# Optimization experiments

Measured on AMD Instinct MI355X. Metric: run time of the kernel, lower is better.

The kernel has to match this reference:

```python
import jax, jax.numpy as jnp
import numpy as np

NB, H, NH, R, C, V, B = 4, 256, 8, 20, 128, 32, 2
P = R * (R - 1) // 2  # 190 pairs


def _pair_matrix(rows):
    # each row of the mask has exactly two ones (a row pair); equals torch.combinations scatter
    i, j = np.triu_indices(rows, k=1)
    m = np.zeros((len(i), rows), np.float32)
    m[np.arange(len(i)), i] = 1.0
    m[np.arange(len(i)), j] = 1.0
    return jnp.asarray(m)


def setup_inputs() -> dict:
    key = jax.random.key(0)
    ks = jax.random.split(key, 16)

    def n(k, shape, s=0.02):
        return jax.random.normal(k, shape, jnp.float32) * s

    return {
        "tokens": jax.random.randint(ks[0], (B, R, C), 0, V, dtype=jnp.int32),
        "emb": n(ks[1], (V, H), 1.0),
        "ln1_g": jnp.ones((NB, H)), "ln1_b": jnp.zeros((NB, H)),
        "rWq": n(ks[2], (NB, H, H)), "rWk": n(ks[3], (NB, H, H)),
        "rWv": n(ks[4], (NB, H, H)), "rWo": n(ks[5], (NB, H, H)),
        "ln2_g": jnp.ones((NB, H)), "ln2_b": jnp.zeros((NB, H)),
        "cWq": n(ks[6], (NB, H, H)), "cWk": n(ks[7], (NB, H, H)),
        "cWv": n(ks[8], (NB, H, H)), "cWo": n(ks[9], (NB, H, H)),
        "ln3_g": jnp.ones((NB, H)), "ln3_b": jnp.zeros((NB, H)),
        "fW1": n(ks[10], (NB, H, 4 * H)), "fb1": jnp.zeros((NB, 4 * H)),
        "fW2": n(ks[11], (NB, 4 * H, H)), "fb2": jnp.zeros((NB, H)),
        "pW1": n(ks[12], (H, 4 * H)), "pb1": jnp.zeros((4 * H,)),
        "pW2": n(ks[13], (4 * H, 1)), "pb2": jnp.zeros((1,)),
        "uW": n(ks[14], (C, 1)), "ub": jnp.zeros((1,)),
    }


def _layernorm(x, g, b, eps=1e-5):
    m = x.mean(-1, keepdims=True)
    v = x.var(-1, keepdims=True)
    return (x - m) * jax.lax.rsqrt(v + eps) * g + b


def _attn(x, Wq, Wk, Wv, Wo):
    # x: [B, A, L, H]; multi-head attention over axis L
    b, a, l, h = x.shape
    d = h // NH
    q = (x @ Wq).reshape(b, a, l, NH, d)
    k = (x @ Wk).reshape(b, a, l, NH, d)
    v = (x @ Wv).reshape(b, a, l, NH, d)
    s = jnp.einsum('balhd,bamhd->bahlm', q, k) * (1.0 / float(np.sqrt(d)))
    p = jax.nn.softmax(s, axis=-1)
    o = jnp.einsum('bahlm,bamhd->balhd', p, v).reshape(b, a, l, h)
    return o @ Wo


def reference(tokens, emb, ln1_g, ln1_b, rWq, rWk, rWv, rWo, ln2_g, ln2_b, cWq, cWk, cWv, cWo, ln3_g, ln3_b, fW1, fb1, fW2, fb2, pW1, pb1, pW2, pb2, uW, ub):
    pm = _pair_matrix(tokens.shape[1])           # [P, R]
    x = emb[tokens]                              # [B, R, C, H]
    x = jnp.einsum('pr,brch->bpch', pm, x)       # pairwise row-sum -> [B, P, C, H]
    for i in range(ln1_g.shape[0]):
        h = _layernorm(x, ln1_g[i], ln1_b[i])
        x = x + _attn(h.swapaxes(1, 2), rWq[i], rWk[i], rWv[i], rWo[i]).swapaxes(1, 2)  # attend over pair axis
        h = _layernorm(x, ln2_g[i], ln2_b[i])
        x = x + _attn(h, cWq[i], cWk[i], cWv[i], cWo[i])                                # attend over column axis
        h = _layernorm(x, ln3_g[i], ln3_b[i])
        x = x + jax.nn.gelu(h @ fW1[i] + fb1[i]) @ fW2[i] + fb2[i]
    y = (jax.nn.gelu(x @ pW1 + pb1) @ pW2 + pb2).squeeze(-1)  # [B, P, C]
    y = (y @ uW + ub).squeeze(-1)                              # [B, P]
    return y
```

## Files before the change

kernel.cpp:

```cpp
#include <hip/hip_runtime.h>
#include <hip/hip_bf16.h>
#include <stdint.h>

#define NBLK   4
#define HDIM   256
#define NHEADS 8
#define RDIM   20
#define CDIM   128
#define PDIM   190
#define BDIM   2
#define FDIM   1024
#define NROWS  (BDIM*PDIM*CDIM)
#define NF     ((size_t)NROWS*(size_t)HDIM)
#define HROWS  (NROWS/2)

typedef __attribute__((ext_vector_type(8))) short bf16x8;
typedef __attribute__((ext_vector_type(4))) float f32x4;

__device__ __forceinline__ short f2b(float f){
    uint32_t u = __float_as_uint(f);
    u += 0x7fff + ((u >> 16) & 1);
    return (short)(u >> 16);
}
__device__ __forceinline__ float b2f(short s){
    return __uint_as_float(((uint32_t)(uint16_t)s) << 16);
}
__device__ __forceinline__ float gelu_tanh(float x){
    const float k0 = 0.7978845608028654f;
    const float k1 = 0.044715f;
    return 0.5f*x*(1.0f + tanhf(k0*(x + k1*x*x*x)));
}
__device__ __forceinline__ void async16(const void* g, void* l){
    __builtin_amdgcn_global_load_lds(
        (const __attribute__((address_space(1))) void*)g,
        (__attribute__((address_space(3))) void*)l, 16, 0, 0);
}

__global__ __launch_bounds__(256) void embed_kernel(
    const int* __restrict__ tokens, const float* __restrict__ emb,
    float* __restrict__ x)
{
    int n    = blockIdx.x*4 + (threadIdx.x >> 6);
    int lane = threadIdx.x & 63;
    int c  = n % CDIM;
    int bp = n / CDIM;
    int p  = bp % PDIM;
    int b  = bp / PDIM;
    int i = 0, rem = p;
    while (rem >= (RDIM - 1 - i)) { rem -= (RDIM - 1 - i); ++i; }
    int j = i + 1 + rem;
    int t1 = tokens[(b*RDIM + i)*CDIM + c];
    int t2 = tokens[(b*RDIM + j)*CDIM + c];
    float4 e1 = *(const float4*)(emb + (size_t)t1*HDIM + lane*4);
    float4 e2 = *(const float4*)(emb + (size_t)t2*HDIM + lane*4);
    float4 o; o.x = e1.x+e2.x; o.y = e1.y+e2.y; o.z = e1.z+e2.z; o.w = e1.w+e2.w;
    *(float4*)(x + (size_t)n*HDIM + lane*4) = o;
}

__global__ __launch_bounds__(256) void ln_kernel(
    const float* __restrict__ X, const float* __restrict__ g,
    const float* __restrict__ bta, short* __restrict__ Out)
{
    int row  = blockIdx.x*4 + (threadIdx.x >> 6);
    int lane = threadIdx.x & 63;
    float4 v = *(const float4*)(X + (size_t)row*HDIM + lane*4);
    float s1 = v.x + v.y + v.z + v.w;
    float s2 = v.x*v.x + v.y*v.y + v.z*v.z + v.w*v.w;
    #pragma unroll
    for (int off = 1; off < 64; off <<= 1) {
        s1 += __shfl_xor(s1, off);
        s2 += __shfl_xor(s2, off);
    }
    float mu  = s1 * (1.0f/HDIM);
    float var = s2 * (1.0f/HDIM) - mu*mu;
    float inv = rsqrtf(var + 1e-5f);
    float4 gg = *(const float4*)(g   + lane*4);
    float4 bb = *(const float4*)(bta + lane*4);
    short4 o;
    o.x = f2b((v.x - mu)*inv*gg.x + bb.x);
    o.y = f2b((v.y - mu)*inv*gg.y + bb.y);
    o.z = f2b((v.z - mu)*inv*gg.z + bb.z);
    o.w = f2b((v.w - mu)*inv*gg.w + bb.w);
    *(short4*)(Out + (size_t)row*HDIM + lane*4) = o;
}

__global__ __launch_bounds__(256) void cvt4_kernel(
    const float* __restrict__ in, short* __restrict__ out)
{
    size_t i = (size_t)blockIdx.x*256 + threadIdx.x;
    float4 f = ((const float4*)in)[i];
    short4 s;
    s.x = f2b(f.x); s.y = f2b(f.y); s.z = f2b(f.z); s.w = f2b(f.w);
    ((short4*)out)[i] = s;
}

__global__ __launch_bounds__(256) void tconv_kernel(
    const float* __restrict__ in, short* __restrict__ out,
    int K, int M, size_t inz, size_t outz)
{
    __shared__ float t[32][33];
    in  += (size_t)blockIdx.z * inz;
    out += (size_t)blockIdx.z * outz;
    int m0 = blockIdx.x*32, k0 = blockIdx.y*32;
    int r = threadIdx.x >> 5, c = threadIdx.x & 31;
    #pragma unroll
    for (int i = 0; i < 4; ++i)
        t[r + i*8][c] = in[(size_t)(k0 + r + i*8)*M + m0 + c];
    __syncthreads();
    #pragma unroll
    for (int i = 0; i < 4; ++i) {
        int rr = r + i*8;
        out[(size_t)(m0 + rr)*K + k0 + c] = f2b(t[c][rr]);
    }
}

template<int EPI>
__global__ __launch_bounds__(256) void mgemm_kernel(
    const short* __restrict__ A, const short* __restrict__ Wt,
    const float* __restrict__ bias,
    float* __restrict__ OutF,
    short* __restrict__ OB0, short* __restrict__ OB1, short* __restrict__ OB2,
    int K, int M)
{
    __shared__ short As[2][128*32];
    __shared__ short Bs[2][128*32];
    const int tid  = threadIdx.x;
    const int lane = tid & 63, wid = tid >> 6;
    const int lq = lane & 15, lk = lane >> 4;
    const int wr = wid >> 1, wc = wid & 1;
    const int row0 = blockIdx.y * 128, col0 = blockIdx.x * 128;

    f32x4 acc[4][4] = {};

    auto stage = [&](int buf, int k0) {
        #pragma unroll
        for (int u = 0; u < 2; ++u) {
            int b   = wid*1024 + lane*16 + u*4096;
            int r   = b >> 6;
            int c16 = (b >> 4) & 3;
            int cs  = (c16 ^ (r & 3)) * 8;
            async16(A  + (size_t)(row0 + r)*K + k0 + cs, (char*)As[buf] + b);
            async16(Wt + (size_t)(col0 + r)*K + k0 + cs, (char*)Bs[buf] + b);
        }
    };

    stage(0, 0);
    const int NTK = K >> 5;
    for (int t = 0; t < NTK; ++t) {
        const int cur = t & 1;
        asm volatile("s_waitcnt vmcnt(0)" ::: "memory");
        __builtin_amdgcn_s_barrier();
        __builtin_amdgcn_sched_barrier(0);
        if (t + 1 < NTK) stage(cur ^ 1, (t + 1)*32);

        bf16x8 af[4], bfr[4];
        #pragma unroll
        for (int m = 0; m < 4; ++m) {
            int row = wr*64 + m*16 + lq;
            af[m] = *(const bf16x8*)((const char*)As[cur] + row*64 + ((lk ^ (lq & 3)) << 4));
        }
        #pragma unroll
        for (int n = 0; n < 4; ++n) {
            int row = wc*64 + n*16 + lq;
            bfr[n] = *(const bf16x8*)((const char*)Bs[cur] + row*64 + ((lk ^ (lq & 3)) << 4));
        }
        #pragma unroll
        for (int m = 0; m < 4; ++m)
            #pragma unroll
            for (int n = 0; n < 4; ++n)
                acc[m][n] = __builtin_amdgcn_mfma_f32_16x16x32_bf16(af[m], bfr[n], acc[m][n], 0, 0, 0);
    }

    const int rb  = row0 + wr*64 + (lk << 2);
    const int cb0 = col0 + wc*64 + lq;
    #pragma unroll
    for (int m = 0; m < 4; ++m) {
        #pragma unroll
        for (int n = 0; n < 4; ++n) {
            int col = cb0 + n*16;
            #pragma unroll
            for (int r = 0; r < 4; ++r) {
                int row = rb + m*16 + r;
                float vv = acc[m][n][r];
                if (EPI == 0) {
                    int sec = col >> 8, cc = col & 255;
                    short* o = (sec == 0) ? OB0 : ((sec == 1) ? OB1 : OB2);
                    o[(size_t)row*HDIM + cc] = f2b(vv);
                } else if (EPI == 1) {
                    OutF[(size_t)row*HDIM + col] += vv;
                } else if (EPI == 2) {
                    OB0[(size_t)row*M + col] = f2b(gelu_tanh(vv + bias[col]));
                } else {
                    OutF[(size_t)row*HDIM + col] += vv + bias[col];
                }
            }
        }
    }
}

template<int LP>
__global__ __launch_bounds__(256) void attn_mfma(
    const short* __restrict__ Q, const short* __restrict__ K,
    const short* __restrict__ V, short* __restrict__ O,
    int Lreal, int isRow)
{
    constexpr int NT  = LP/16;
    constexpr int NKT = LP/32;
    constexpr int NCH = LP/64;
    constexpr int LPB = LP*2;

    __shared__ short Ks[LP*32];
    __shared__ short Vt[32*LP];
    __shared__ short Ps[4*16*LP];

    const int bid  = blockIdx.x;
    const int head = bid & 7;
    size_t base; int S;
    if (isRow) {
        int c = (bid >> 3) & (CDIM-1);
        int b = bid >> 10;
        base = ((size_t)b*PDIM*CDIM + c)*HDIM + head*32;
        S = CDIM*HDIM;
    } else {
        int p = (bid >> 3) % PDIM;
        int b = bid / (8*PDIM);
        base = ((size_t)(b*PDIM + p)*CDIM)*HDIM + head*32;
        S = HDIM;
    }

    const int tid  = threadIdx.x;
    const int lane = tid & 63, wid = tid >> 6;
    const int lq = lane & 15, lk = lane >> 4;

    #pragma unroll
    for (int it = 0; it < LP/64; ++it) {
        int t16 = it*256 + tid;
        int row = t16 >> 2;
        int rc  = row < Lreal ? row : Lreal-1;
        async16((const char*)K + (base + (size_t)rc*S + (t16 & 3)*8)*2,
                (char*)Ks + (size_t)t16*16);
    }
    #pragma unroll
    for (int it = 0; it < LP/32; ++it) {
        int e   = it*256 + tid;
        int row = e >> 3;
        int d4  = (e & 7)*4;
        int rc  = row < Lreal ? row : Lreal-1;
        short4 v4 = *(const short4*)(V + base + (size_t)rc*S + d4);
        #pragma unroll
        for (int j = 0; j < 4; ++j) {
            int d = d4 + j;
            int off = ((d*LP + row)*2) ^ ((d & 7) << 4);
            *(short*)((char*)Vt + off) = ((const short*)&v4)[j];
        }
    }
    __syncthreads();

    const float scale = 0.17677669529663687f;
    char* pbase = (char*)Ps + wid*(16*LPB);
    const f32x4 zero = {0.f, 0.f, 0.f, 0.f};

    #pragma unroll 1
    for (int cc = 0; cc < NCH; ++cc) {
        const int chunk = wid + cc*4;
        const int qrow0 = chunk*16;

        int qr = qrow0 + lq; if (qr >= Lreal) qr = Lreal-1;
        bf16x8 qa = *(const bf16x8*)(Q + base + (size_t)qr*S + lk*8);

        f32x4 s[NT];
        #pragma unroll
        for (int t = 0; t < NT; ++t) {
            bf16x8 kb = *(const bf16x8*)(Ks + (t*16 + lq)*32 + lk*8);
            s[t] = __builtin_amdgcn_mfma_f32_16x16x32_bf16(qa, kb, zero, 0, 0, 0);
        }
        if ((NT-1)*16 + lq >= Lreal) {
            #pragma unroll
            for (int r = 0; r < 4; ++r) s[NT-1][r] = -1e30f;
        }
        float mx[4] = {-1e30f, -1e30f, -1e30f, -1e30f};
        #pragma unroll
        for (int t = 0; t < NT; ++t)
            #pragma unroll
            for (int r = 0; r < 4; ++r) mx[r] = fmaxf(mx[r], s[t][r]);
        #pragma unroll
        for (int off = 1; off < 16; off <<= 1)
            #pragma unroll
            for (int r = 0; r < 4; ++r) mx[r] = fmaxf(mx[r], __shfl_xor(mx[r], off));
        float sm[4] = {0.f, 0.f, 0.f, 0.f};
        #pragma unroll
        for (int t = 0; t < NT; ++t)
            #pragma unroll
            for (int r = 0; r < 4; ++r) {
                float p = __expf((s[t][r] - mx[r])*scale);
                s[t][r] = p; sm[r] += p;
            }
        #pragma unroll
        for (int off = 1; off < 16; off <<= 1)
            #pragma unroll
            for (int r = 0; r < 4; ++r) sm[r] += __shfl_xor(sm[r], off);

        #pragma unroll
        for (int t = 0; t < NT; ++t)
            #pragma unroll
            for (int r = 0; r < 4; ++r) {
                int row = lk*4 + r, col = t*16 + lq;
                int off = (row*LPB + col*2) ^ ((row & 7) << 4);
                *(short*)(pbase + off) = f2b(s[t][r]);
            }
        asm volatile("s_waitcnt lgkmcnt(0)" ::: "memory");
        __builtin_amdgcn_sched_barrier(0);

        f32x4 acc0 = zero, acc1 = zero;
        #pragma unroll
        for (int kt = 0; kt < NKT; ++kt) {
            bf16x8 pa = *(const bf16x8*)(pbase + ((lq*LPB + kt*64 + lk*16) ^ ((lq & 7) << 4)));
            bf16x8 v0 = *(const bf16x8*)((char*)Vt + ((lq*LPB      + kt*64 + lk*16) ^ ((lq & 7) << 4)));
            bf16x8 v1 = *(const bf16x8*)((char*)Vt + (((16+lq)*LPB + kt*64 + lk*16) ^ ((lq & 7) << 4)));
            acc0 = __builtin_amdgcn_mfma_f32_16x16x32_bf16(pa, v0, acc0, 0, 0, 0);
            acc1 = __builtin_amdgcn_mfma_f32_16x16x32_bf16(pa, v1, acc1, 0, 0, 0);
        }
        __builtin_amdgcn_sched_barrier(0);

        #pragma unroll
        for (int r = 0; r < 4; ++r) {
            int row = qrow0 + lk*4 + r;
            if (row < Lreal) {
                float inv = 1.0f / sm[r];
                O[base + (size_t)row*S + lq]      = f2b(acc0[r]*inv);
                O[base + (size_t)row*S + 16 + lq] = f2b(acc1[r]*inv);
            }
        }
    }
}

__global__ __launch_bounds__(256) void gemv_head(
    const short* __restrict__ T, const float* __restrict__ w,
    const float* __restrict__ bias, float* __restrict__ y)
{
    int row  = blockIdx.x*4 + (threadIdx.x >> 6);
    int lane = threadIdx.x & 63;
    const short* t = T + (size_t)row*FDIM;
    float acc = 0.f;
    #pragma unroll
    for (int it = 0; it < 4; ++it) {
        int ci = it*64 + lane;
        short4 tv = *(const short4*)(t + ci*4);
        float4 wv = *(const float4*)(w + ci*4);
        acc += b2f(tv.x)*wv.x + b2f(tv.y)*wv.y + b2f(tv.z)*wv.z + b2f(tv.w)*wv.w;
    }
    #pragma unroll
    for (int off = 1; off < 64; off <<= 1) acc += __shfl_xor(acc, off);
    if (lane == 0) y[row] = acc + bias[0];
}

__global__ __launch_bounds__(128) void final_kernel(
    const float* __restrict__ y, const float* __restrict__ uW,
    const float* __restrict__ ub, float* __restrict__ out)
{
    int bp = blockIdx.x;
    int c  = threadIdx.x;
    float v = y[(size_t)bp*CDIM + c]*uW[c];
    #pragma unroll
    for (int off = 1; off < 64; off <<= 1) v += __shfl_xor(v, off);
    __shared__ float r[2];
    if ((c & 63) == 0) r[c >> 6] = v;
    __syncthreads();
    if (c == 0) out[bp] = r[0] + r[1] + ub[0];
}

extern "C" void kernel_launch(void* const* d_in, const int* in_sizes, int n_in,
                              void* d_out, int out_size, void* d_ws, size_t ws_size,
                              hipStream_t stream)
{
    const int*   tokens = (const int*)  d_in[0];
    const float* emb    = (const float*)d_in[1];
    const float* ln1_g  = (const float*)d_in[2];
    const float* ln1_b  = (const float*)d_in[3];
    const float* rWq    = (const float*)d_in[4];
    const float* rWk    = (const float*)d_in[5];
    const float* rWv    = (const float*)d_in[6];
    const float* rWo    = (const float*)d_in[7];
    const float* ln2_g  = (const float*)d_in[8];
    const float* ln2_b  = (const float*)d_in[9];
    const float* cWq    = (const float*)d_in[10];
    const float* cWk    = (const float*)d_in[11];
    const float* cWv    = (const float*)d_in[12];
    const float* cWo    = (const float*)d_in[13];
    const float* ln3_g  = (const float*)d_in[14];
    const float* ln3_b  = (const float*)d_in[15];
    const float* fW1    = (const float*)d_in[16];
    const float* fb1    = (const float*)d_in[17];
    const float* fW2    = (const float*)d_in[18];
    const float* fb2    = (const float*)d_in[19];
    const float* pW1    = (const float*)d_in[20];
    const float* pb1    = (const float*)d_in[21];
    const float* pW2    = (const float*)d_in[22];
    const float* pb2    = (const float*)d_in[23];
    const float* uW     = (const float*)d_in[24];
    const float* ub     = (const float*)d_in[25];

    float* x  = (float*)d_ws;
    short* q  = (short*)(x + NF);
    short* k  = q + NF;
    short* v  = k + NF;
    short* hb = v + NF;
    float* y  = (float*)(hb + NF);
    short* wts = (short*)(y + NROWS);
    short* w_rqkv = wts;
    short* w_cqkv = w_rqkv + 4*768*256;
    short* w_ro   = w_cqkv + 4*768*256;
    short* w_co   = w_ro   + 4*256*256;
    short* w_f1   = w_co   + 4*256*256;
    short* w_f2   = w_f1   + (size_t)4*1024*256;
    short* w_p1   = w_f2   + (size_t)4*1024*256;
    short* tb = q;

    const size_t HH = 65536, HF = 262144, QZ = 768*256;

    tconv_kernel<<<dim3(8,8,NBLK),   256, 0, stream>>>(rWq, w_rqkv,          256, 256,  HH, QZ);
    tconv_kernel<<<dim3(8,8,NBLK),   256, 0, stream>>>(rWk, w_rqkv + 65536,  256, 256,  HH, QZ);
    tconv_kernel<<<dim3(8,8,NBLK),   256, 0, stream>>>(rWv, w_rqkv + 131072, 256, 256,  HH, QZ);
    tconv_kernel<<<dim3(8,8,NBLK),   256, 0, stream>>>(rWo, w_ro,            256, 256,  HH, HH);
    tconv_kernel<<<dim3(8,8,NBLK),   256, 0, stream>>>(cWq, w_cqkv,          256, 256,  HH, QZ);
    tconv_kernel<<<dim3(8,8,NBLK),   256, 0, stream>>>(cWk, w_cqkv + 65536,  256, 256,  HH, QZ);
    tconv_kernel<<<dim3(8,8,NBLK),   256, 0, stream>>>(cWv, w_cqkv + 131072, 256, 256,  HH, QZ);
    tconv_kernel<<<dim3(8,8,NBLK),   256, 0, stream>>>(cWo, w_co,            256, 256,  HH, HH);
    tconv_kernel<<<dim3(32,8,NBLK),  256, 0, stream>>>(fW1, w_f1,            256, 1024, HF, HF);
    tconv_kernel<<<dim3(8,32,NBLK),  256, 0, stream>>>(fW2, w_f2,            1024, 256, HF, HF);
    tconv_kernel<<<dim3(32,8,1),     256, 0, stream>>>(pW1, w_p1,            256, 1024, HF, HF);

    embed_kernel<<<NROWS/4, 256, 0, stream>>>(tokens, emb, x);

    const dim3 gQKV(6, NROWS/128);
    const dim3 gO(2, NROWS/128);
    const dim3 gF1(8, HROWS/128);
    const dim3 gF2(2, HROWS/128);

    for (int i = 0; i < NBLK; ++i) {
        ln_kernel<<<NROWS/4, 256, 0, stream>>>(x, ln1_g + i*HDIM, ln1_b + i*HDIM, hb);
        mgemm_kernel<0><<<gQKV, 256, 0, stream>>>(hb, w_rqkv + (size_t)i*QZ, nullptr, nullptr, q, k, v, 256, 768);
        attn_mfma<192><<<BDIM*CDIM*NHEADS, 256, 0, stream>>>(q, k, v, hb, PDIM, 1);
        mgemm_kernel<1><<<gO, 256, 0, stream>>>(hb, w_ro + i*HH, nullptr, x, nullptr, nullptr, nullptr, 256, 256);

        ln_kernel<<<NROWS/4, 256, 0, stream>>>(x, ln2_g + i*HDIM, ln2_b + i*HDIM, hb);
        mgemm_kernel<0><<<gQKV, 256, 0, stream>>>(hb, w_cqkv + (size_t)i*QZ, nullptr, nullptr, q, k, v, 256, 768);
        attn_mfma<128><<<BDIM*PDIM*NHEADS, 256, 0, stream>>>(q, k, v, hb, CDIM, 0);
        mgemm_kernel<1><<<gO, 256, 0, stream>>>(hb, w_co + i*HH, nullptr, x, nullptr, nullptr, nullptr, 256, 256);

        ln_kernel<<<NROWS/4, 256, 0, stream>>>(x, ln3_g + i*HDIM, ln3_b + i*HDIM, hb);
        for (int ch = 0; ch < 2; ++ch) {
            mgemm_kernel<2><<<gF1, 256, 0, stream>>>(hb + (size_t)ch*HROWS*HDIM, w_f1 + (size_t)i*HF,
                                                     fb1 + i*FDIM, nullptr, tb, nullptr, nullptr, 256, 1024);
            mgemm_kernel<3><<<gF2, 256, 0, stream>>>(tb, w_f2 + (size_t)i*HF,
                                                     fb2 + i*HDIM, x + (size_t)ch*HROWS*HDIM,
                                                     nullptr, nullptr, nullptr, 1024, 256);
        }
    }

    cvt4_kernel<<<NF/4/256, 256, 0, stream>>>(x, hb);
    for (int ch = 0; ch < 2; ++ch) {
        mgemm_kernel<2><<<gF1, 256, 0, stream>>>(hb + (size_t)ch*HROWS*HDIM, w_p1, pb1,
                                                 nullptr, tb, nullptr, nullptr, 256, 1024);
        gemv_head<<<HROWS/4, 256, 0, stream>>>(tb, pW2, pb2, y + (size_t)ch*HROWS);
    }
    final_kernel<<<BDIM*PDIM, 128, 0, stream>>>(y, uW, ub, (float*)d_out);
}
```

Measured before the change: 1.787 ms.

## Fuse LayerNorm into residual GEMM epilogues and triple-buffer GEMM loads

Residual-adding GEMMs (attention output projections and the second FFN matmul) now compute a full 256-wide row tile per block. In the epilogue they add bias and residual into x, then reduce mean and variance across waves through shared memory and write the next LayerNorm's bf16 output. This removes the standalone LN kernels and the final fp32-to-bf16 conversion pass, and the embedding is fused with the first LN. The generic GEMM also moves from double to triple buffering with a partial vmcnt wait. The trade-off is fewer, heavier blocks with a larger accumulator (more register pressure, less occupancy) and more LDS.

```diff
diff --git a/kernel.cpp b/kernel.cpp
--- a/kernel.cpp
+++ b/kernel.cpp
@@ -36,9 +36,10 @@
         (__attribute__((address_space(3))) void*)l, 16, 0, 0);
 }
 
-__global__ __launch_bounds__(256) void embed_kernel(
+__global__ __launch_bounds__(256) void embed_ln_kernel(
     const int* __restrict__ tokens, const float* __restrict__ emb,
-    float* __restrict__ x)
+    const float* __restrict__ g, const float* __restrict__ bta,
+    float* __restrict__ x, short* __restrict__ hb)
 {
     int n    = blockIdx.x*4 + (threadIdx.x >> 6);
     int lane = threadIdx.x & 63;
@@ -53,17 +54,9 @@
     int t2 = tokens[(b*RDIM + j)*CDIM + c];
     float4 e1 = *(const float4*)(emb + (size_t)t1*HDIM + lane*4);
     float4 e2 = *(const float4*)(emb + (size_t)t2*HDIM + lane*4);
-    float4 o; o.x = e1.x+e2.x; o.y = e1.y+e2.y; o.z = e1.z+e2.z; o.w = e1.w+e2.w;
-    *(float4*)(x + (size_t)n*HDIM + lane*4) = o;
-}
-
-__global__ __launch_bounds__(256) void ln_kernel(
-    const float* __restrict__ X, const float* __restrict__ g,
-    const float* __restrict__ bta, short* __restrict__ Out)
-{
-    int row  = blockIdx.x*4 + (threadIdx.x >> 6);
-    int lane = threadIdx.x & 63;
-    float4 v = *(const float4*)(X + (size_t)row*HDIM + lane*4);
+    float4 v; v.x = e1.x+e2.x; v.y = e1.y+e2.y; v.z = e1.z+e2.z; v.w = e1.w+e2.w;
+    *(float4*)(x + (size_t)n*HDIM + lane*4) = v;
+
     float s1 = v.x + v.y + v.z + v.w;
     float s2 = v.x*v.x + v.y*v.y + v.z*v.z + v.w*v.w;
     #pragma unroll
@@ -81,17 +74,7 @@
     o.y = f2b((v.y - mu)*inv*gg.y + bb.y);
     o.z = f2b((v.z - mu)*inv*gg.z + bb.z);
     o.w = f2b((v.w - mu)*inv*gg.w + bb.w);
-    *(short4*)(Out + (size_t)row*HDIM + lane*4) = o;
-}
-
-__global__ __launch_bounds__(256) void cvt4_kernel(
-    const float* __restrict__ in, short* __restrict__ out)
-{
-    size_t i = (size_t)blockIdx.x*256 + threadIdx.x;
-    float4 f = ((const float4*)in)[i];
-    short4 s;
-    s.x = f2b(f.x); s.y = f2b(f.y); s.z = f2b(f.z); s.w = f2b(f.w);
-    ((short4*)out)[i] = s;
+    *(short4*)(hb + (size_t)n*HDIM + lane*4) = o;
 }
 
 __global__ __launch_bounds__(256) void tconv_kernel(
@@ -118,12 +101,11 @@
 __global__ __launch_bounds__(256) void mgemm_kernel(
     const short* __restrict__ A, const short* __restrict__ Wt,
     const float* __restrict__ bias,
-    float* __restrict__ OutF,
     short* __restrict__ OB0, short* __restrict__ OB1, short* __restrict__ OB2,
     int K, int M)
 {
-    __shared__ short As[2][128*32];
-    __shared__ short Bs[2][128*32];
+    __shared__ short As[3][128*32];
+    __shared__ short Bs[3][128*32];
     const int tid  = threadIdx.x;
     const int lane = tid & 63, wid = tid >> 6;
     const int lq = lane & 15, lk = lane >> 4;
@@ -141,6 +123,96 @@
             int cs  = (c16 ^ (r & 3)) * 8;
             async16(A  + (size_t)(row0 + r)*K + k0 + cs, (char*)As[buf] + b);
             async16(Wt + (size_t)(col0 + r)*K + k0 + cs, (char*)Bs[buf] + b);
+        }
+    };
+
+    const int NTK = K >> 5;
+    stage(0, 0);
+    stage(1, 32);
+    for (int t = 0; t < NTK; ++t) {
+        const int cur = t % 3;
+        asm volatile("s_waitcnt vmcnt(4)" ::: "memory");
+        __builtin_amdgcn_s_barrier();
+        __builtin_amdgcn_sched_barrier(0);
+        int tn = t + 2; if (tn >= NTK) tn = NTK - 1;
+        stage((t + 2) % 3, tn*32);
+
+        bf16x8 af[4], bfr[4];
+        #pragma unroll
+        for (int m = 0; m < 4; ++m) {
+            int row = wr*64 + m*16 + lq;
+            af[m] = *(const bf16x8*)((const char*)As[cur] + row*64 + ((lk ^ (lq & 3)) << 4));
+        }
+        #pragma unroll
+        for (int n = 0; n < 4; ++n) {
+            int row = wc*64 + n*16 + lq;
+            bfr[n] = *(const bf16x8*)((const char*)Bs[cur] + row*64 + ((lk ^ (lq & 3)) << 4));
+        }
+        #pragma unroll
+        for (int m = 0; m < 4; ++m)
+            #pragma unroll
+            for (int n = 0; n < 4; ++n)
+                acc[m][n] = __builtin_amdgcn_mfma_f32_16x16x32_bf16(af[m], bfr[n], acc[m][n], 0, 0, 0);
+    }
+
+    const int rb  = row0 + wr*64 + (lk << 2);
+    const int cb0 = col0 + wc*64 + lq;
+    #pragma unroll
+    for (int m = 0; m < 4; ++m) {
+        #pragma unroll
+        for (int n = 0; n < 4; ++n) {
+            int col = cb0 + n*16;
+            #pragma unroll
+            for (int r = 0; r < 4; ++r) {
+                int row = rb + m*16 + r;
+                float vv = acc[m][n][r];
+                if (EPI == 0) {
+                    int sec = col >> 8, cc = col & 255;
+                    short* o = (sec == 0) ? OB0 : ((sec == 1) ? OB1 : OB2);
+                    o[(size_t)row*HDIM + cc] = f2b(vv);
+                } else {
+                    OB0[(size_t)row*M + col] = f2b(gelu_tanh(vv + bias[col]));
+                }
+            }
+        }
+    }
+}
+
+template<int MODE>
+__global__ __launch_bounds__(256) void mgemm_ln_kernel(
+    const short* __restrict__ A, const short* __restrict__ Wt,
+    const float* __restrict__ bias,
+    float* __restrict__ OutF, short* __restrict__ OB,
+    const float* __restrict__ lng, const float* __restrict__ lnb,
+    int K)
+{
+    __shared__ short As[2][128*32];
+    __shared__ short Bs[2][256*32];
+    __shared__ float red[2][2][64][2];
+    const int tid  = threadIdx.x;
+    const int lane = tid & 63, wid = tid >> 6;
+    const int lq = lane & 15, lk = lane >> 4;
+    const int wr = wid >> 1, wc = wid & 1;
+    const int row0 = blockIdx.x * 128;
+
+    f32x4 acc[4][8] = {};
+
+    auto stage = [&](int buf, int k0) {
+        #pragma unroll
+        for (int u = 0; u < 2; ++u) {
+            int b   = wid*1024 + lane*16 + u*4096;
+            int r   = b >> 6;
+            int c16 = (b >> 4) & 3;
+            int cs  = (c16 ^ (r & 3)) * 8;
+            async16(A + (size_t)(row0 + r)*K + k0 + cs, (char*)As[buf] + b);
+        }
+        #pragma unroll
+        for (int u = 0; u < 4; ++u) {
+            int b   = wid*1024 + lane*16 + u*4096;
+            int r   = b >> 6;
+            int c16 = (b >> 4) & 3;
+            int cs  = (c16 ^ (r & 3)) * 8;
+            async16(Wt + (size_t)r*K + k0 + cs, (char*)Bs[buf] + b);
         }
     };
 
@@ -153,46 +225,105 @@
         __builtin_amdgcn_sched_barrier(0);
         if (t + 1 < NTK) stage(cur ^ 1, (t + 1)*32);
 
-        bf16x8 af[4], bfr[4];
+        bf16x8 af[4], bfr[8];
         #pragma unroll
         for (int m = 0; m < 4; ++m) {
             int row = wr*64 + m*16 + lq;
             af[m] = *(const bf16x8*)((const char*)As[cur] + row*64 + ((lk ^ (lq & 3)) << 4));
         }
         #pragma unroll
-        for (int n = 0; n < 4; ++n) {
-            int row = wc*64 + n*16 + lq;
+        for (int n = 0; n < 8; ++n) {
+            int row = wc*128 + n*16 + lq;
             bfr[n] = *(const bf16x8*)((const char*)Bs[cur] + row*64 + ((lk ^ (lq & 3)) << 4));
         }
         #pragma unroll
         for (int m = 0; m < 4; ++m)
             #pragma unroll
-            for (int n = 0; n < 4; ++n)
+            for (int n = 0; n < 8; ++n)
                 acc[m][n] = __builtin_amdgcn_mfma_f32_16x16x32_bf16(af[m], bfr[n], acc[m][n], 0, 0, 0);
     }
 
-    const int rb  = row0 + wr*64 + (lk << 2);
-    const int cb0 = col0 + wc*64 + lq;
+    float bias8[8];
+    #pragma unroll
+    for (int n = 0; n < 8; ++n)
+        bias8[n] = (MODE >= 1) ? bias[wc*128 + n*16 + lq] : 0.0f;
+
     #pragma unroll
     for (int m = 0; m < 4; ++m) {
         #pragma unroll
-        for (int n = 0; n < 4; ++n) {
-            int col = cb0 + n*16;
+        for (int r = 0; r < 4; ++r) {
+            int row = row0 + wr*64 + m*16 + lk*4 + r;
+            #pragma unroll
+            for (int n = 0; n < 8; ++n) {
+                int col = wc*128 + n*16 + lq;
+                float vv = acc[m][n][r] + bias8[n] + OutF[(size_t)row*HDIM + col];
+                OutF[(size_t)row*HDIM + col] = vv;
+                acc[m][n][r] = vv;
+            }
+        }
+    }
+
+    if (MODE == 2) {
+        #pragma unroll
+        for (int m = 0; m < 4; ++m)
             #pragma unroll
             for (int r = 0; r < 4; ++r) {
-                int row = rb + m*16 + r;
-                float vv = acc[m][n][r];
-                if (EPI == 0) {
-                    int sec = col >> 8, cc = col & 255;
-                    short* o = (sec == 0) ? OB0 : ((sec == 1) ? OB1 : OB2);
-                    o[(size_t)row*HDIM + cc] = f2b(vv);
-                } else if (EPI == 1) {
-                    OutF[(size_t)row*HDIM + col] += vv;
-                } else if (EPI == 2) {
-                    OB0[(size_t)row*M + col] = f2b(gelu_tanh(vv + bias[col]));
-                } else {
-                    OutF[(size_t)row*HDIM + col] += vv + bias[col];
+                int row = row0 + wr*64 + m*16 + lk*4 + r;
+                #pragma unroll
+                for (int n = 0; n < 8; ++n) {
+                    int col = wc*128 + n*16 + lq;
+                    OB[(size_t)row*HDIM + col] = f2b(acc[m][n][r]);
                 }
+            }
+        return;
+    }
+
+    #pragma unroll
+    for (int m = 0; m < 4; ++m) {
+        #pragma unroll
+        for (int r = 0; r < 4; ++r) {
+            float a = 0.f, b = 0.f;
+            #pragma unroll
+            for (int n = 0; n < 8; ++n) {
+                float v = acc[m][n][r];
+                a += v; b += v*v;
+            }
+            #pragma unroll
+            for (int off = 1; off < 16; off <<= 1) {
+                a += __shfl_xor(a, off);
+                b += __shfl_xor(b, off);
+            }
+            if (lq == 0) {
+                int r64 = m*16 + lk*4 + r;
+                red[wc][wr][r64][0] = a;
+                red[wc][wr][r64][1] = b;
+            }
+        }
+    }
+    __syncthreads();
+
+    float g8[8], bb8[8];
+    #pragma unroll
+    for (int n = 0; n < 8; ++n) {
+        int col = wc*128 + n*16 + lq;
+        g8[n]  = lng[col];
+        bb8[n] = lnb[col];
+    }
+    #pragma unroll
+    for (int m = 0; m < 4; ++m) {
+        #pragma unroll
+        for (int r = 0; r < 4; ++r) {
+            int r64 = m*16 + lk*4 + r;
+            float sum = red[0][wr][r64][0] + red[1][wr][r64][0];
+            float sq  = red[0][wr][r64][1] + red[1][wr][r64][1];
+            float mu  = sum * (1.0f/HDIM);
+            float var = sq * (1.0f/HDIM) - mu*mu;
+            float inv = rsqrtf(var + 1e-5f);
+            int row = row0 + wr*64 + m*16 + lk*4 + r;
+            #pragma unroll
+            for (int n = 0; n < 8; ++n) {
+                int col = wc*128 + n*16 + lq;
+                OB[(size_t)row*HDIM + col] = f2b((acc[m][n][r] - mu)*inv*g8[n] + bb8[n]);
             }
         }
     }
@@ -430,38 +561,40 @@
     tconv_kernel<<<dim3(8,32,NBLK),  256, 0, stream>>>(fW2, w_f2,            1024, 256, HF, HF);
     tconv_kernel<<<dim3(32,8,1),     256, 0, stream>>>(pW1, w_p1,            256, 1024, HF, HF);
 
-    embed_kernel<<<NROWS/4, 256, 0, stream>>>(tokens, emb, x);
+    embed_ln_kernel<<<NROWS/4, 256, 0, stream>>>(tokens, emb, ln1_g, ln1_b, x, hb);
 
     const dim3 gQKV(6, NROWS/128);
-    const dim3 gO(2, NROWS/128);
     const dim3 gF1(8, HROWS/128);
-    const dim3 gF2(2, HROWS/128);
 
     for (int i = 0; i < NBLK; ++i) {
-        ln_kernel<<<NROWS/4, 256, 0, stream>>>(x, ln1_g + i*HDIM, ln1_b + i*HDIM, hb);
-        mgemm_kernel<0><<<gQKV, 256, 0, stream>>>(hb, w_rqkv + (size_t)i*QZ, nullptr, nullptr, q, k, v, 256, 768);
+        mgemm_kernel<0><<<gQKV, 256, 0, stream>>>(hb, w_rqkv + (size_t)i*QZ, nullptr, q, k, v, 256, 768);
         attn_mfma<192><<<BDIM*CDIM*NHEADS, 256, 0, stream>>>(q, k, v, hb, PDIM, 1);
-        mgemm_kernel<1><<<gO, 256, 0, stream>>>(hb, w_ro + i*HH, nullptr, x, nullptr, nullptr, nullptr, 256, 256);
-
-        ln_kernel<<<NROWS/4, 256, 0, stream>>>(x, ln2_g + i*HDIM, ln2_b + i*HDIM, hb);
-        mgemm_kernel<0><<<gQKV, 256, 0, stream>>>(hb, w_cqkv + (size_t)i*QZ, nullptr, nullptr, q, k, v, 256, 768);
+        mgemm_ln_kernel<0><<<NROWS/128, 256, 0, stream>>>(hb, w_ro + i*HH, nullptr, x, hb,
+                                                          ln2_g + i*HDIM, ln2_b + i*HDIM, 256);
+
+        mgemm_kernel<0><<<gQKV, 256, 0, stream>>>(hb, w_cqkv + (size_t)i*QZ, nullptr, q, k, v, 256, 768);
         attn_mfma<128><<<BDIM*PDIM*NHEADS, 256, 0, stream>>>(q, k, v, hb, CDIM, 0);
-        mgemm_kernel<1><<<gO, 256, 0, stream>>>(hb, w_co + i*HH, nullptr, x, nullptr, nullptr, nullptr, 256, 256);
-
-        ln_kernel<<<NROWS/4, 256, 0, stream>>>(x, ln3_g + i*HDIM, ln3_b + i*HDIM, hb);
+        mgemm_ln_kernel<0><<<NROWS/128, 256, 0, stream>>>(hb, w_co + i*HH, nullptr, x, hb,
+                                                          ln3_g + i*HDIM, ln3_b + i*HDIM, 256);
+
         for (int ch = 0; ch < 2; ++ch) {
-            mgemm_kernel<2><<<gF1, 256, 0, stream>>>(hb + (size_t)ch*HROWS*HDIM, w_f1 + (size_t)i*HF,
-                                                     fb1 + i*FDIM, nullptr, tb, nullptr, nullptr, 256, 1024);
-            mgemm_kernel<3><<<gF2, 256, 0, stream>>>(tb, w_f2 + (size_t)i*HF,
-                                                     fb2 + i*HDIM, x + (size_t)ch*HROWS*HDIM,
-                                                     nullptr, nullptr, nullptr, 1024, 256);
-        }
-    }
-
-    cvt4_kernel<<<NF/4/256, 256, 0, stream>>>(x, hb);
+            const size_t ro = (size_t)ch*HROWS*HDIM;
+            mgemm_kernel<2><<<gF1, 256, 0, stream>>>(hb + ro, w_f1 + (size_t)i*HF,
+                                                     fb1 + i*FDIM, tb, nullptr, nullptr, 256, 1024);
+            if (i < NBLK-1)
+                mgemm_ln_kernel<1><<<HROWS/128, 256, 0, stream>>>(tb, w_f2 + (size_t)i*HF,
+                                                                  fb2 + i*HDIM, x + ro, hb + ro,
+                                                                  ln1_g + (i+1)*HDIM, ln1_b + (i+1)*HDIM, 1024);
+            else
+                mgemm_ln_kernel<2><<<HROWS/128, 256, 0, stream>>>(tb, w_f2 + (size_t)i*HF,
+                                                                  fb2 + i*HDIM, x + ro, hb + ro,
+                                                                  nullptr, nullptr, 1024);
+        }
+    }
+
     for (int ch = 0; ch < 2; ++ch) {
-        mgemm_kernel<2><<<gF1, 256, 0, stream>>>(hb + (size_t)ch*HROWS*HDIM, w_p1, pb1,
-                                                 nullptr, tb, nullptr, nullptr, 256, 1024);
+        const size_t ro = (size_t)ch*HROWS*HDIM;
+        mgemm_kernel<2><<<gF1, 256, 0, stream>>>(hb + ro, w_p1, pb1, tb, nullptr, nullptr, 256, 1024);
         gemv_head<<<HROWS/4, 256, 0, stream>>>(tb, pW2, pb2, y + (size_t)ch*HROWS);
     }
     final_kernel<<<BDIM*PDIM, 128, 0, stream>>>(y, uW, ub, (float*)d_out);
```

Result: slower. 1.968 ms (+10.1%).

## Fuse first layernorm into embed, swizzle K tile in LDS, use packed bf16 convert

Applied to the files above, without the earlier changes.

The embedding kernel now also computes the first block's layernorm and writes the bf16 normalized activations, so the first ln_kernel launch and its re-read of x are skipped. In the attention kernel, K is loaded into LDS with an XOR swizzle on 16-byte chunks to reduce bank conflicts on the MFMA operand reads. Manual float-to-bf16 rounding is replaced by the hardware v_cvt_pk_bf16_f32 instruction. These are small savings against a workload dominated by GEMMs.

```diff
diff --git a/kernel.cpp b/kernel.cpp
--- a/kernel.cpp
+++ b/kernel.cpp
@@ -25,6 +25,11 @@
 __device__ __forceinline__ float b2f(short s){
     return __uint_as_float(((uint32_t)(uint16_t)s) << 16);
 }
+__device__ __forceinline__ int cvtpk(float a, float b){
+    int r;
+    asm("v_cvt_pk_bf16_f32 %0, %1, %2" : "=v"(r) : "v"(a), "v"(b));
+    return r;
+}
 __device__ __forceinline__ float gelu_tanh(float x){
     const float k0 = 0.7978845608028654f;
     const float k1 = 0.044715f;
@@ -36,9 +41,10 @@
         (__attribute__((address_space(3))) void*)l, 16, 0, 0);
 }
 
-__global__ __launch_bounds__(256) void embed_kernel(
+__global__ __launch_bounds__(256) void embed_ln_kernel(
     const int* __restrict__ tokens, const float* __restrict__ emb,
-    float* __restrict__ x)
+    const float* __restrict__ g, const float* __restrict__ bta,
+    float* __restrict__ x, short* __restrict__ hb)
 {
     int n    = blockIdx.x*4 + (threadIdx.x >> 6);
     int lane = threadIdx.x & 63;
@@ -53,8 +59,27 @@
     int t2 = tokens[(b*RDIM + j)*CDIM + c];
     float4 e1 = *(const float4*)(emb + (size_t)t1*HDIM + lane*4);
     float4 e2 = *(const float4*)(emb + (size_t)t2*HDIM + lane*4);
-    float4 o; o.x = e1.x+e2.x; o.y = e1.y+e2.y; o.z = e1.z+e2.z; o.w = e1.w+e2.w;
-    *(float4*)(x + (size_t)n*HDIM + lane*4) = o;
+    float4 v; v.x = e1.x+e2.x; v.y = e1.y+e2.y; v.z = e1.z+e2.z; v.w = e1.w+e2.w;
+    *(float4*)(x + (size_t)n*HDIM + lane*4) = v;
+
+    float s1 = v.x + v.y + v.z + v.w;
+    float s2 = v.x*v.x + v.y*v.y + v.z*v.z + v.w*v.w;
+    #pragma unroll
+    for (int off = 1; off < 64; off <<= 1) {
+        s1 += __shfl_xor(s1, off);
+        s2 += __shfl_xor(s2, off);
+    }
+    float mu  = s1 * (1.0f/HDIM);
+    float var = s2 * (1.0f/HDIM) - mu*mu;
+    float inv = rsqrtf(var + 1e-5f);
+    float4 gg = *(const float4*)(g   + lane*4);
+    float4 bb = *(const float4*)(bta + lane*4);
+    short4 o;
+    o.x = f2b((v.x - mu)*inv*gg.x + bb.x);
+    o.y = f2b((v.y - mu)*inv*gg.y + bb.y);
+    o.z = f2b((v.z - mu)*inv*gg.z + bb.z);
+    o.w = f2b((v.w - mu)*inv*gg.w + bb.w);
+    *(short4*)(hb + (size_t)n*HDIM + lane*4) = o;
 }
 
 __global__ __launch_bounds__(256) void ln_kernel(
@@ -237,8 +262,8 @@
         int t16 = it*256 + tid;
         int row = t16 >> 2;
         int rc  = row < Lreal ? row : Lreal-1;
-        async16((const char*)K + (base + (size_t)rc*S + (t16 & 3)*8)*2,
-                (char*)Ks + (size_t)t16*16);
+        int cs  = ((t16 & 3) ^ (row & 3)) * 8;
+        async16(K + base + (size_t)rc*S + cs, (char*)Ks + (size_t)t16*16);
     }
     #pragma unroll
     for (int it = 0; it < LP/32; ++it) {
@@ -271,7 +296,7 @@
         f32x4 s[NT];
         #pragma unroll
         for (int t = 0; t < NT; ++t) {
-            bf16x8 kb = *(const bf16x8*)(Ks + (t*16 + lq)*32 + lk*8);
+            bf16x8 kb = *(const bf16x8*)((const char*)Ks + (t*16 + lq)*64 + ((lk ^ (lq & 3)) << 4));
             s[t] = __builtin_amdgcn_mfma_f32_16x16x32_bf16(qa, kb, zero, 0, 0, 0);
         }
         if ((NT-1)*16 + lq >= Lreal) {
@@ -306,7 +331,7 @@
             for (int r = 0; r < 4; ++r) {
                 int row = lk*4 + r, col = t*16 + lq;
                 int off = (row*LPB + col*2) ^ ((row & 7) << 4);
-                *(short*)(pbase + off) = f2b(s[t][r]);
+                *(short*)(pbase + off) = (short)cvtpk(s[t][r], s[t][r]);
             }
         asm volatile("s_waitcnt lgkmcnt(0)" ::: "memory");
         __builtin_amdgcn_sched_barrier(0);
@@ -327,8 +352,8 @@
             int row = qrow0 + lk*4 + r;
             if (row < Lreal) {
                 float inv = 1.0f / sm[r];
-                O[base + (size_t)row*S + lq]      = f2b(acc0[r]*inv);
-                O[base + (size_t)row*S + 16 + lq] = f2b(acc1[r]*inv);
+                O[base + (size_t)row*S + lq]      = (short)cvtpk(acc0[r]*inv, acc0[r]*inv);
+                O[base + (size_t)row*S + 16 + lq] = (short)cvtpk(acc1[r]*inv, acc1[r]*inv);
             }
         }
     }
@@ -430,7 +455,7 @@
     tconv_kernel<<<dim3(8,32,NBLK),  256, 0, stream>>>(fW2, w_f2,            1024, 256, HF, HF);
     tconv_kernel<<<dim3(32,8,1),     256, 0, stream>>>(pW1, w_p1,            256, 1024, HF, HF);
 
-    embed_kernel<<<NROWS/4, 256, 0, stream>>>(tokens, emb, x);
+    embed_ln_kernel<<<NROWS/4, 256, 0, stream>>>(tokens, emb, ln1_g, ln1_b, x, hb);
 
     const dim3 gQKV(6, NROWS/128);
     const dim3 gO(2, NROWS/128);
@@ -438,7 +463,8 @@
     const dim3 gF2(2, HROWS/128);
 
     for (int i = 0; i < NBLK; ++i) {
-        ln_kernel<<<NROWS/4, 256, 0, stream>>>(x, ln1_g + i*HDIM, ln1_b + i*HDIM, hb);
+        if (i > 0)
+            ln_kernel<<<NROWS/4, 256, 0, stream>>>(x, ln1_g + i*HDIM, ln1_b + i*HDIM, hb);
         mgemm_kernel<0><<<gQKV, 256, 0, stream>>>(hb, w_rqkv + (size_t)i*QZ, nullptr, nullptr, q, k, v, 256, 768);
         attn_mfma<192><<<BDIM*CDIM*NHEADS, 256, 0, stream>>>(q, k, v, hb, PDIM, 1);
         mgemm_kernel<1><<<gO, 256, 0, stream>>>(hb, w_ro + i*HH, nullptr, x, nullptr, nullptr, nullptr, 256, 256);
```

After: 1.773 ms. Within noise of the previous version (-0.8%).
